# Optimization experiments

Hardware: AMD Instinct MI355X
Metric: run time of the kernel (lower is better)

The kernel has to match this reference:

```python
import jax, jax.numpy as jnp
import numpy as np

DICE_W = 0.5
CHAMFER_W = 0.5
SMOOTH = 1e-6


def setup_inputs() -> dict:
    key = jax.random.key(0)
    k1, k2, k3, k4 = jax.random.split(key, 4)
    B, H, W = 4, 1024, 1024
    N = M = 8192
    predictions = jax.random.normal(k1, (B, 1, H, W), dtype=jnp.float32)   # logits
    target = jax.random.uniform(k2, (B, 1, H, W), dtype=jnp.float32)       # soft GT mask
    pred_points = jax.random.normal(k3, (1, N, 2), dtype=jnp.float32)      # pred boundary pts
    target_points = jax.random.normal(k4, (1, M, 2), dtype=jnp.float32)    # GT boundary pts
    return {"predictions": predictions, "target": target,
            "pred_points": pred_points, "target_points": target_points}


def _dice_loss(pred_logits, target):
    pred = jax.nn.sigmoid(pred_logits)
    intersection = jnp.sum(pred * target)
    union = jnp.sum(pred) + jnp.sum(target)
    dice = (2.0 * intersection + SMOOTH) / (union + SMOOTH)
    return 1.0 - dice


def _chamfer_loss(pred_points, target_points):
    # pairwise squared distances: (1, N, M)
    diff = pred_points[:, :, None, :] - target_points[:, None, :, :]
    d2 = jnp.sum(diff * diff, axis=-1)
    # bidirectional chamfer: mean of nearest-neighbor sq-dist in each direction
    return jnp.mean(jnp.min(d2, axis=2)) + jnp.mean(jnp.min(d2, axis=1))


def reference(predictions, target, pred_points, target_points):
    dice = _dice_loss(predictions, target)
    chamfer = _chamfer_loss(pred_points, target_points)
    return DICE_W * dice + CHAMFER_W * chamfer
```

## Files before the change

### kernel.cpp

```cpp
#include <hip/hip_runtime.h>
#include <math.h>

#define INFBITS 0x7F800000u
#define TCH 128
#define PTS 8
#define DICE_BLOCKS 512

typedef float v2f __attribute__((ext_vector_type(2)));

__device__ __forceinline__ float block_sum256(float v) {
#pragma unroll
    for (int o = 32; o > 0; o >>= 1) v += __shfl_down(v, o, 64);
    __shared__ float sb[4];
    if ((threadIdx.x & 63) == 0) sb[threadIdx.x >> 6] = v;
    __syncthreads();
    float r = sb[0] + sb[1] + sb[2] + sb[3];
    __syncthreads();
    return r;
}

__global__ void __launch_bounds__(256) fused_partials(
        const float4* __restrict__ p4, const float4* __restrict__ t4, int n4,
        float* __restrict__ inter_p, float* __restrict__ uni_p,
        const float2* __restrict__ P, const float2* __restrict__ T,
        int N, int M, float* __restrict__ pm, int npm, int chm, int gxp,
        unsigned int* __restrict__ counter) {
    int bid = blockIdx.x;
    if (bid == 0 && threadIdx.x == 0) *counter = 0u;

    if (bid < DICE_BLOCKS) {
        float inter = 0.f, uni = 0.f;
#pragma unroll 2
        for (int i = bid * 256 + threadIdx.x; i < n4; i += DICE_BLOCKS * 256) {
            float4 p = p4[i];
            float4 t = t4[i];
            float s;
            s = __fdividef(1.f, 1.f + __expf(-p.x)); inter = fmaf(s, t.x, inter); uni += s + t.x;
            s = __fdividef(1.f, 1.f + __expf(-p.y)); inter = fmaf(s, t.y, inter); uni += s + t.y;
            s = __fdividef(1.f, 1.f + __expf(-p.z)); inter = fmaf(s, t.z, inter); uni += s + t.z;
            s = __fdividef(1.f, 1.f + __expf(-p.w)); inter = fmaf(s, t.w, inter); uni += s + t.w;
        }
        float bi = block_sum256(inter);
        float bu = block_sum256(uni);
        if (threadIdx.x == 0) { inter_p[bid] = bi; uni_p[bid] = bu; }
        return;
    }

    int cb      = bid - DICE_BLOCKS;
    int per_dir = gxp * chm;
    int dir     = cb / per_dir;
    int rem     = cb - dir * per_dir;
    int cy      = rem / gxp;
    int cx      = rem - cy * gxp;
    const float2* A = dir ? T : P;
    const float2* B = dir ? P : T;
    int nA = dir ? M : N;
    int nB = dir ? N : M;

    int tb = cy * TCH;
    if (tb >= nB) return;

    __shared__ __align__(16) float4 qs[TCH / 2];
    int t = threadIdx.x;
    if (t < TCH / 2) {
        int j0 = tb + 2 * t;
        float4 r = make_float4(1e18f, 1e18f, 1e18f, 1e18f);
        if (j0 + 1 < nB) {
            float4 b = *(const float4*)&B[j0];
            r = make_float4(b.x, b.z, b.y, b.w);
        } else if (j0 < nB) {
            float2 b = B[j0];
            r = make_float4(b.x, 1e18f, b.y, 1e18f);
        }
        qs[t] = r;
    }
    __syncthreads();

    int abase = cx * (PTS * 256);
    v2f nx2[PTS], ny2[PTS];
    float mn[PTS];
#pragma unroll
    for (int i = 0; i < PTS; ++i) {
        int p = abase + i * 256 + t;
        float nx = 0.f, ny = 0.f;
        mn[i] = __uint_as_float(INFBITS);
        if (p < nA) {
            float2 a = A[p];
            nx = -2.f * a.x;
            ny = -2.f * a.y;
        }
        nx2[i] = (v2f){nx, nx};
        ny2[i] = (v2f){ny, ny};
    }

#pragma unroll 4
    for (int jp = 0; jp < TCH / 2; ++jp) {
        float4 q = qs[jp];
        v2f X = (v2f){q.x, q.y};
        v2f Y = (v2f){q.z, q.w};
        v2f S = X * X + Y * Y;
#pragma unroll
        for (int i = 0; i < PTS; ++i) {
            v2f D = nx2[i] * X + (ny2[i] * Y + S);
            mn[i] = fminf(fminf(mn[i], D.x), D.y);
        }
    }

    float* dstc = pm + ((size_t)dir * chm + cy) * npm;
#pragma unroll
    for (int i = 0; i < PTS; ++i) {
        int p = abase + i * 256 + t;
        if (p < nA) dstc[p] = mn[i];
    }
}

__global__ void __launch_bounds__(256) finalize_all(
        const float* __restrict__ pm, int npm, int chm,
        int N, int M, int nch0, int nch1,
        const float2* __restrict__ P, const float2* __restrict__ T,
        const float* __restrict__ inter_p, const float* __restrict__ uni_p,
        float* __restrict__ bsum, unsigned int* __restrict__ counter,
        int gxf, float* __restrict__ out) {
    int blk = blockIdx.x;
    int dir = blk / gxf;
    int bx  = blk - dir * gxf;
    int nA  = dir ? M : N;
    int nch = dir ? nch1 : nch0;
    const float2* A = dir ? T : P;

    int p = bx * 256 + threadIdx.x;
    float v = 0.f;
    if (p < nA) {
        const float* src = pm + (size_t)dir * chm * npm + p;
        float m = __uint_as_float(INFBITS);
#pragma unroll 16
        for (int c = 0; c < nch; ++c) m = fminf(m, src[(size_t)c * npm]);
        float2 a = A[p];
        v = m + fmaf(a.x, a.x, a.y * a.y);
    }
    float s = block_sum256(v);

    __shared__ int is_last;
    if (threadIdx.x == 0) {
        bsum[blk] = s;
        __threadfence();
        unsigned int old = atomicAdd(counter, 1u);
        is_last = (old == (unsigned)(2 * gxf - 1));
    }
    __syncthreads();
    if (!is_last) return;
    __threadfence();

    float inter = 0.f, uni = 0.f, c0 = 0.f, c1 = 0.f;
    for (int i = threadIdx.x; i < DICE_BLOCKS; i += 256) {
        inter += inter_p[i];
        uni   += uni_p[i];
    }
    const volatile float* vb = bsum;
    for (int i = threadIdx.x; i < gxf; i += 256) {
        c0 += vb[i];
        c1 += vb[gxf + i];
    }
    float bi  = block_sum256(inter);
    float bu  = block_sum256(uni);
    float bc0 = block_sum256(c0);
    float bc1 = block_sum256(c1);
    if (threadIdx.x == 0) {
        const float SMOOTH = 1e-6f;
        float dice    = (2.f * bi + SMOOTH) / (bu + SMOOTH);
        float chamfer = bc0 / (float)N + bc1 / (float)M;
        out[0] = 0.5f * (1.f - dice) + 0.5f * chamfer;
    }
}

extern "C" void kernel_launch(void* const* d_in, const int* in_sizes, int n_in,
                              void* d_out, int out_size, void* d_ws, size_t ws_size,
                              hipStream_t stream) {
    const float*  pred = (const float*)d_in[0];
    const float*  targ = (const float*)d_in[1];
    const float2* pp   = (const float2*)d_in[2];
    const float2* tp   = (const float2*)d_in[3];
    int n = in_sizes[0];
    int N = in_sizes[2] / 2;
    int M = in_sizes[3] / 2;
    float* out = (float*)d_out;

    int npm  = N > M ? N : M;
    int nch0 = (M + TCH - 1) / TCH;
    int nch1 = (N + TCH - 1) / TCH;
    int chm  = nch0 > nch1 ? nch0 : nch1;
    int gxp  = (npm + PTS * 256 - 1) / (PTS * 256);
    int gxf  = (npm + 255) / 256;

    char*  ws      = (char*)d_ws;
    float* pm      = (float*)ws;
    size_t pm_bytes = (size_t)2 * chm * npm * sizeof(float);
    size_t off     = (pm_bytes + 255) & ~(size_t)255;
    float* inter_p = (float*)(ws + off);
    float* uni_p   = inter_p + DICE_BLOCKS;
    float* bsum    = uni_p + DICE_BLOCKS;
    unsigned int* counter = (unsigned int*)(bsum + 2 * gxf);

    int cham_blocks = 2 * gxp * chm;
    fused_partials<<<DICE_BLOCKS + cham_blocks, 256, 0, stream>>>(
        (const float4*)pred, (const float4*)targ, n / 4,
        inter_p, uni_p, pp, tp, N, M, pm, npm, chm, gxp, counter);

    finalize_all<<<2 * gxf, 256, 0, stream>>>(pm, npm, chm, N, M, nch0, nch1,
                                              pp, tp, inter_p, uni_p, bsum,
                                              counter, gxf, out);
}
```

Baseline: 28.38 us.

## Fuse finalize into single kernel using atomic counters and spin-wait grid sync

Merges the separate finalize kernel into the main kernel. The first 64 chamfer blocks spin-wait on a global counter until every chamfer tile has written its partial minima, then perform the column-min scan, and the last scanning block waits for the dice blocks and writes the output. This removes one kernel launch and the gap between kernels, but it adds a memset launch and relies on all spinning blocks being co-resident. Launch bounds with a min-blocks hint are also added to raise occupancy.

```diff
diff --git a/kernel.cpp b/kernel.cpp
--- a/kernel.cpp
+++ b/kernel.cpp
@@ -5,6 +5,8 @@
 #define TCH 128
 #define PTS 8
 #define DICE_BLOCKS 512
+#define SCAN_PER_DIR 32
+#define SCAN_BLOCKS (2 * SCAN_PER_DIR)
 
 typedef float v2f __attribute__((ext_vector_type(2)));
 
@@ -19,30 +21,38 @@
     return r;
 }
 
-__global__ void __launch_bounds__(256) fused_partials(
+__global__ void __launch_bounds__(256, 4) fused_one(
         const float4* __restrict__ p4, const float4* __restrict__ t4, int n4,
         float* __restrict__ inter_p, float* __restrict__ uni_p,
         const float2* __restrict__ P, const float2* __restrict__ T,
         int N, int M, float* __restrict__ pm, int npm, int chm, int gxp,
-        unsigned int* __restrict__ counter) {
+        int cham_blocks, int nch0, int nch1,
+        float* __restrict__ bsum,
+        unsigned int* __restrict__ cnt_dice,
+        unsigned int* __restrict__ cnt_cham,
+        unsigned int* __restrict__ cnt_scan,
+        float* __restrict__ out) {
     int bid = blockIdx.x;
-    if (bid == 0 && threadIdx.x == 0) *counter = 0u;
+    int t   = threadIdx.x;
 
     if (bid < DICE_BLOCKS) {
         float inter = 0.f, uni = 0.f;
 #pragma unroll 2
-        for (int i = bid * 256 + threadIdx.x; i < n4; i += DICE_BLOCKS * 256) {
+        for (int i = bid * 256 + t; i < n4; i += DICE_BLOCKS * 256) {
             float4 p = p4[i];
-            float4 t = t4[i];
+            float4 tt = t4[i];
             float s;
-            s = __fdividef(1.f, 1.f + __expf(-p.x)); inter = fmaf(s, t.x, inter); uni += s + t.x;
-            s = __fdividef(1.f, 1.f + __expf(-p.y)); inter = fmaf(s, t.y, inter); uni += s + t.y;
-            s = __fdividef(1.f, 1.f + __expf(-p.z)); inter = fmaf(s, t.z, inter); uni += s + t.z;
-            s = __fdividef(1.f, 1.f + __expf(-p.w)); inter = fmaf(s, t.w, inter); uni += s + t.w;
+            s = __fdividef(1.f, 1.f + __expf(-p.x)); inter = fmaf(s, tt.x, inter); uni += s + tt.x;
+            s = __fdividef(1.f, 1.f + __expf(-p.y)); inter = fmaf(s, tt.y, inter); uni += s + tt.y;
+            s = __fdividef(1.f, 1.f + __expf(-p.z)); inter = fmaf(s, tt.z, inter); uni += s + tt.z;
+            s = __fdividef(1.f, 1.f + __expf(-p.w)); inter = fmaf(s, tt.w, inter); uni += s + tt.w;
         }
         float bi = block_sum256(inter);
         float bu = block_sum256(uni);
-        if (threadIdx.x == 0) { inter_p[bid] = bi; uni_p[bid] = bu; }
+        if (t == 0) { inter_p[bid] = bi; uni_p[bid] = bu; }
+        __threadfence();
+        __syncthreads();
+        if (t == 0) atomicAdd(cnt_dice, 1u);
         return;
     }
 
@@ -52,120 +62,129 @@
     int rem     = cb - dir * per_dir;
     int cy      = rem / gxp;
     int cx      = rem - cy * gxp;
-    const float2* A = dir ? T : P;
-    const float2* B = dir ? P : T;
-    int nA = dir ? M : N;
-    int nB = dir ? N : M;
-
-    int tb = cy * TCH;
-    if (tb >= nB) return;
-
-    __shared__ __align__(16) float4 qs[TCH / 2];
-    int t = threadIdx.x;
-    if (t < TCH / 2) {
-        int j0 = tb + 2 * t;
-        float4 r = make_float4(1e18f, 1e18f, 1e18f, 1e18f);
-        if (j0 + 1 < nB) {
-            float4 b = *(const float4*)&B[j0];
-            r = make_float4(b.x, b.z, b.y, b.w);
-        } else if (j0 < nB) {
-            float2 b = B[j0];
-            r = make_float4(b.x, 1e18f, b.y, 1e18f);
-        }
-        qs[t] = r;
-    }
-    __syncthreads();
-
-    int abase = cx * (PTS * 256);
-    v2f nx2[PTS], ny2[PTS];
-    float mn[PTS];
-#pragma unroll
-    for (int i = 0; i < PTS; ++i) {
-        int p = abase + i * 256 + t;
-        float nx = 0.f, ny = 0.f;
-        mn[i] = __uint_as_float(INFBITS);
+    {
+        const float2* A = dir ? T : P;
+        const float2* B = dir ? P : T;
+        int nA = dir ? M : N;
+        int nB = dir ? N : M;
+
+        int tb = cy * TCH;
+        if (tb < nB) {
+            __shared__ __align__(16) float4 qs[TCH / 2];
+            if (t < TCH / 2) {
+                int j0 = tb + 2 * t;
+                float4 r = make_float4(1e18f, 1e18f, 1e18f, 1e18f);
+                if (j0 + 1 < nB) {
+                    float4 b = *(const float4*)&B[j0];
+                    r = make_float4(b.x, b.z, b.y, b.w);
+                } else if (j0 < nB) {
+                    float2 b = B[j0];
+                    r = make_float4(b.x, 1e18f, b.y, 1e18f);
+                }
+                qs[t] = r;
+            }
+            __syncthreads();
+
+            int abase = cx * (PTS * 256);
+            v2f nx2[PTS], ny2[PTS];
+            float mn[PTS];
+#pragma unroll
+            for (int i = 0; i < PTS; ++i) {
+                int p = abase + i * 256 + t;
+                float nx = 0.f, ny = 0.f;
+                mn[i] = __uint_as_float(INFBITS);
+                if (p < nA) {
+                    float2 a = A[p];
+                    nx = -2.f * a.x;
+                    ny = -2.f * a.y;
+                }
+                nx2[i] = (v2f){nx, nx};
+                ny2[i] = (v2f){ny, ny};
+            }
+
+#pragma unroll 4
+            for (int jp = 0; jp < TCH / 2; ++jp) {
+                float4 q = qs[jp];
+                v2f X = (v2f){q.x, q.y};
+                v2f Y = (v2f){q.z, q.w};
+                v2f S = X * X + Y * Y;
+#pragma unroll
+                for (int i = 0; i < PTS; ++i) {
+                    v2f D = nx2[i] * X + (ny2[i] * Y + S);
+                    mn[i] = fminf(fminf(mn[i], D.x), D.y);
+                }
+            }
+
+            float* dstc = pm + ((size_t)dir * chm + cy) * npm;
+#pragma unroll
+            for (int i = 0; i < PTS; ++i) {
+                int p = abase + i * 256 + t;
+                if (p < nA) dstc[p] = mn[i];
+            }
+        }
+    }
+    __threadfence();
+    __syncthreads();
+    if (t == 0) atomicAdd(cnt_cham, 1u);
+
+    if (cb >= SCAN_BLOCKS) return;
+
+    if (t == 0) {
+        while (atomicAdd(cnt_cham, 0u) < (unsigned)cham_blocks)
+            __builtin_amdgcn_s_sleep(32);
+    }
+    __syncthreads();
+    __threadfence();
+
+    {
+        int sdir = cb / SCAN_PER_DIR;
+        int bx   = cb - sdir * SCAN_PER_DIR;
+        int nA   = sdir ? M : N;
+        int nch  = sdir ? nch1 : nch0;
+        const float2* A = sdir ? T : P;
+
+        int p = bx * 256 + t;
+        float v = 0.f;
         if (p < nA) {
+            const float* src = pm + (size_t)sdir * chm * npm + p;
+            float m = __uint_as_float(INFBITS);
+#pragma unroll 16
+            for (int c = 0; c < nch; ++c) m = fminf(m, src[(size_t)c * npm]);
             float2 a = A[p];
-            nx = -2.f * a.x;
-            ny = -2.f * a.y;
-        }
-        nx2[i] = (v2f){nx, nx};
-        ny2[i] = (v2f){ny, ny};
-    }
-
-#pragma unroll 4
-    for (int jp = 0; jp < TCH / 2; ++jp) {
-        float4 q = qs[jp];
-        v2f X = (v2f){q.x, q.y};
-        v2f Y = (v2f){q.z, q.w};
-        v2f S = X * X + Y * Y;
-#pragma unroll
-        for (int i = 0; i < PTS; ++i) {
-            v2f D = nx2[i] * X + (ny2[i] * Y + S);
-            mn[i] = fminf(fminf(mn[i], D.x), D.y);
-        }
-    }
-
-    float* dstc = pm + ((size_t)dir * chm + cy) * npm;
-#pragma unroll
-    for (int i = 0; i < PTS; ++i) {
-        int p = abase + i * 256 + t;
-        if (p < nA) dstc[p] = mn[i];
-    }
-}
-
-__global__ void __launch_bounds__(256) finalize_all(
-        const float* __restrict__ pm, int npm, int chm,
-        int N, int M, int nch0, int nch1,
-        const float2* __restrict__ P, const float2* __restrict__ T,
-        const float* __restrict__ inter_p, const float* __restrict__ uni_p,
-        float* __restrict__ bsum, unsigned int* __restrict__ counter,
-        int gxf, float* __restrict__ out) {
-    int blk = blockIdx.x;
-    int dir = blk / gxf;
-    int bx  = blk - dir * gxf;
-    int nA  = dir ? M : N;
-    int nch = dir ? nch1 : nch0;
-    const float2* A = dir ? T : P;
-
-    int p = bx * 256 + threadIdx.x;
-    float v = 0.f;
-    if (p < nA) {
-        const float* src = pm + (size_t)dir * chm * npm + p;
-        float m = __uint_as_float(INFBITS);
-#pragma unroll 16
-        for (int c = 0; c < nch; ++c) m = fminf(m, src[(size_t)c * npm]);
-        float2 a = A[p];
-        v = m + fmaf(a.x, a.x, a.y * a.y);
-    }
-    float s = block_sum256(v);
-
-    __shared__ int is_last;
-    if (threadIdx.x == 0) {
-        bsum[blk] = s;
-        __threadfence();
-        unsigned int old = atomicAdd(counter, 1u);
-        is_last = (old == (unsigned)(2 * gxf - 1));
-    }
-    __syncthreads();
-    if (!is_last) return;
+            v = m + fmaf(a.x, a.x, a.y * a.y);
+        }
+        float s = block_sum256(v);
+        __shared__ int is_last;
+        if (t == 0) {
+            bsum[cb] = s;
+            __threadfence();
+            unsigned int old = atomicAdd(cnt_scan, 1u);
+            is_last = (old == (unsigned)(SCAN_BLOCKS - 1));
+        }
+        __syncthreads();
+        if (!is_last) return;
+    }
+
+    if (t == 0) {
+        while (atomicAdd(cnt_dice, 0u) < (unsigned)DICE_BLOCKS)
+            __builtin_amdgcn_s_sleep(32);
+    }
+    __syncthreads();
     __threadfence();
 
     float inter = 0.f, uni = 0.f, c0 = 0.f, c1 = 0.f;
-    for (int i = threadIdx.x; i < DICE_BLOCKS; i += 256) {
-        inter += inter_p[i];
-        uni   += uni_p[i];
-    }
+    const volatile float* vi = inter_p;
+    const volatile float* vu = uni_p;
+    for (int i = t; i < DICE_BLOCKS; i += 256) { inter += vi[i]; uni += vu[i]; }
     const volatile float* vb = bsum;
-    for (int i = threadIdx.x; i < gxf; i += 256) {
-        c0 += vb[i];
-        c1 += vb[gxf + i];
-    }
+    if (t < SCAN_PER_DIR)          c0 = vb[t];
+    else if (t < SCAN_BLOCKS)      c1 = vb[t];
+
     float bi  = block_sum256(inter);
     float bu  = block_sum256(uni);
     float bc0 = block_sum256(c0);
     float bc1 = block_sum256(c1);
-    if (threadIdx.x == 0) {
+    if (t == 0) {
         const float SMOOTH = 1e-6f;
         float dice    = (2.f * bi + SMOOTH) / (bu + SMOOTH);
         float chamfer = bc0 / (float)N + bc1 / (float)M;
@@ -190,7 +209,7 @@
     int nch1 = (N + TCH - 1) / TCH;
     int chm  = nch0 > nch1 ? nch0 : nch1;
     int gxp  = (npm + PTS * 256 - 1) / (PTS * 256);
-    int gxf  = (npm + 255) / 256;
+    int cham_blocks = 2 * gxp * chm;
 
     char*  ws      = (char*)d_ws;
     float* pm      = (float*)ws;
@@ -199,14 +218,14 @@
     float* inter_p = (float*)(ws + off);
     float* uni_p   = inter_p + DICE_BLOCKS;
     float* bsum    = uni_p + DICE_BLOCKS;
-    unsigned int* counter = (unsigned int*)(bsum + 2 * gxf);
-
-    int cham_blocks = 2 * gxp * chm;
-    fused_partials<<<DICE_BLOCKS + cham_blocks, 256, 0, stream>>>(
+    unsigned int* counters = (unsigned int*)(bsum + SCAN_BLOCKS);
+
+    hipMemsetAsync(counters, 0, 3 * sizeof(unsigned int), stream);
+
+    int nblk = DICE_BLOCKS + cham_blocks;
+    fused_one<<<nblk, 256, 0, stream>>>(
         (const float4*)pred, (const float4*)targ, n / 4,
-        inter_p, uni_p, pp, tp, N, M, pm, npm, chm, gxp, counter);
-
-    finalize_all<<<2 * gxf, 256, 0, stream>>>(pm, npm, chm, N, M, nch0, nch1,
-                                              pp, tp, inter_p, uni_p, bsum,
-                                              counter, gxf, out);
+        inter_p, uni_p, pp, tp, N, M, pm, npm, chm, gxp,
+        cham_blocks, nch0, nch1, bsum,
+        counters + 0, counters + 1, counters + 2, out);
 }
```

After: 111.1 us. +291.6%, slower.
